# Performance work log

Measured on AMD Instinct MI355X. Metric: run time of the kernel, lower is better.

## Reference

```python
import jax, jax.numpy as jnp
import numpy as np

K = 32
D = 64
N_ITER = 10


def setup_inputs() -> dict:
    key = jax.random.key(0)
    k1, k2 = jax.random.split(key)
    B = 65536
    x = jax.random.normal(k1, (B, D), dtype=jnp.float32)
    c = jnp.zeros((K,), dtype=jnp.float32)
    mu = jax.random.normal(k2, (K, D), dtype=jnp.float32) * 0.1
    A = jnp.tile(jnp.eye(D, dtype=jnp.float32)[None], (K, 1, 1))
    alpha = jnp.float32(0.1)
    return {"x": x, "c": c, "mu": mu, "A": A, "alpha": alpha}


def _grad_phi(x, c, mu, A):
    # Precision matrices Sigma_i^{-1} = A_i^T A_i : (k, d, d)
    P = jnp.einsum('kji,kjl->kil', A, A)
    diff = x[:, None, :] - mu[None, :, :]          # (B, k, d)
    Pd = jnp.einsum('kij,bkj->bki', P, diff)       # Sigma^{-1} (x - mu)
    quad = jnp.einsum('bki,bki->bk', diff, Pd)     # (B, k)
    # Analytic gradient of phi(x) = logsumexp_i(c_i - 0.5 q_i):
    # grad = -sum_i softmax_i(c_i - 0.5 q_i) * Sigma_i^{-1}(x - mu_i)
    w = jax.nn.softmax(c[None, :] - 0.5 * quad, axis=1)  # (B, k)
    return -jnp.einsum('bk,bki->bi', w, Pd)


def reference(x, c, mu, A, alpha):
    def step(x_cur, _):
        x_new = x_cur + alpha * _grad_phi(x_cur, c, mu, A)
        return x_new, None
    x_final, _ = jax.lax.scan(step, x, None, length=N_ITER)
    return x_final
```

## Files before the change

kernel.cpp:

```cpp
#include <hip/hip_runtime.h>
#include <hip/hip_bf16.h>


typedef __attribute__((ext_vector_type(4))) float f32x4;
typedef __attribute__((ext_vector_type(16))) float f32x16;
typedef __attribute__((ext_vector_type(8))) short bf16x8;

#define KC 32
#define NITER 10
#define WAVE_SCR 6144

typedef __attribute__((address_space(3))) void as3_void;
typedef __attribute__((address_space(1))) const void as1_cvoid;

static __device__ __forceinline__ void gl_lds16(const void* g, void* l) {
  __builtin_amdgcn_global_load_lds((as1_cvoid*)g, (as3_void*)l, 16, 0, 0);
}

static __device__ __forceinline__ unsigned pk_bf16(float a, float b) {
  __hip_bfloat16 ha = __float2bfloat16(a), hb = __float2bfloat16(b);
  unsigned short ua = *(unsigned short*)&ha, ub = *(unsigned short*)&hb;
  return (unsigned)ua | ((unsigned)ub << 16);
}

__global__ void precompute1(const float* __restrict__ A, const float* __restrict__ mu,
                            const float* __restrict__ c,
                            float* __restrict__ Pmu_g, float* __restrict__ e_g,
                            __hip_bfloat16* __restrict__ Psw) {
  __shared__ float Pk[64 * 64];
  __shared__ float Pmu_s[64];
  const int k = blockIdx.x, tid = threadIdx.x;
  const float* Ak = A + k * 4096;
  for (int idx = tid; idx < 4096; idx += 256) {
    int i = idx >> 6, l = idx & 63;
    float s = 0.f;
    for (int j = 0; j < 64; ++j) s += Ak[j * 64 + i] * Ak[j * 64 + l];
    Pk[idx] = s;
  }
  __syncthreads();
  if (tid < 64) {
    float s = 0.f;
    for (int l = 0; l < 64; ++l) s += Pk[tid * 64 + l] * mu[k * 64 + l];
    Pmu_s[tid] = s;
    Pmu_g[k * 64 + tid] = s;
  }
  __syncthreads();
  if (tid == 0) {
    float s = 0.f;
    for (int i = 0; i < 64; ++i) s += mu[k * 64 + i] * Pmu_s[i];
    e_g[k] = c[k] - 0.5f * s;
  }
  for (int idx = tid; idx < 4096; idx += 256) {
    int f = idx >> 9, lane = (idx >> 3) & 63, j = idx & 7;
    int mt = f >> 2, kf = f & 3, h = lane >> 5, l5 = lane & 31;
    float v = Pk[(kf * 16 + h * 8 + j) * 64 + mt * 32 + l5];
    Psw[k * 4096 + idx] = __float2bfloat16(v);
  }
}

__global__ void precompute2(const float* __restrict__ Pmu_g,
                            __hip_bfloat16* __restrict__ PmuA,
                            __hip_bfloat16* __restrict__ PmuB) {
  const int tid = threadIdx.x;
  for (int idx = tid; idx < 2048; idx += 256) {
    int f = idx >> 9, lane = (idx >> 3) & 63, j = idx & 7;
    int h = lane >> 5, l5 = lane & 31;
    PmuA[idx] = __float2bfloat16(Pmu_g[l5 * 64 + f * 16 + h * 8 + j]);
  }
  for (int idx = tid; idx < 2048; idx += 256) {
    int f = idx >> 9, lane = (idx >> 3) & 63, j = idx & 7;
    int mt = f >> 1, kf = f & 1, h = lane >> 5, l5 = lane & 31;
    PmuB[idx] = __float2bfloat16(Pmu_g[(kf * 16 + h * 8 + j) * 64 + mt * 32 + l5]);
  }
}

__launch_bounds__(256, 2)
__global__ void denoise_main(const float* __restrict__ x_in,
                             const float* __restrict__ e_g,
                             const float* __restrict__ alpha_g,
                             const __hip_bfloat16* __restrict__ Psw,
                             const __hip_bfloat16* __restrict__ PmuA,
                             const __hip_bfloat16* __restrict__ PmuB,
                             float* __restrict__ out) {
  __shared__ __attribute__((aligned(16))) char pbuf[2 * 8192];
  __shared__ __attribute__((aligned(16))) char scratch[4 * WAVE_SCR];

  const int tid = threadIdx.x;
  const int wave = tid >> 6, lane = tid & 63;
  const int h = lane >> 5, l5 = lane & 31;
  const int base_pt = blockIdx.x * 128 + wave * 32;
  const int pt = base_pt + l5;
  const float alpha = alpha_g[0];

  char* sw = scratch + wave * WAVE_SCR;
  float* pmxw = (float*)sw;
  __hip_bfloat16* wtw = (__hip_bfloat16*)(sw + 4096);

  const bf16x8* PmuAF = (const bf16x8*)PmuA;
  const bf16x8* PmuBF = (const bf16x8*)PmuB;

  float xm[2][16];
#pragma unroll
  for (int mt = 0; mt < 2; ++mt)
#pragma unroll
    for (int rq = 0; rq < 4; ++rq) {
      f32x4 v = *(const f32x4*)&x_in[pt * 64 + mt * 32 + rq * 8 + h * 4];
#pragma unroll
      for (int r = 0; r < 4; ++r) xm[mt][rq * 4 + r] = v[r];
    }

  const f32x16 Z16 = {0.f};

#pragma unroll 1
  for (int it = 0; it < NITER; ++it) {
#pragma unroll
    for (int mt = 0; mt < 2; ++mt)
#pragma unroll
      for (int rq = 0; rq < 4; ++rq) {
        unsigned u0 = pk_bf16(xm[mt][rq * 4 + 0], xm[mt][rq * 4 + 1]);
        unsigned u1 = pk_bf16(xm[mt][rq * 4 + 2], xm[mt][rq * 4 + 3]);
        int blk = mt * 4 + rq;
        int addr = l5 * 128 + (((blk) ^ (l5 & 7)) << 4) + 8 * h;
        uint2 v; v.x = u0; v.y = u1;
        *(uint2*)(sw + addr) = v;
      }

    bf16x8 bx[4];
#pragma unroll
    for (int kf = 0; kf < 4; ++kf) {
      int blk = 2 * kf + h;
      bx[kf] = *(const bf16x8*)(sw + l5 * 128 + ((blk ^ (l5 & 7)) << 4));
    }

    {
      const char* g = (const char*)Psw + wave * 2048 + lane * 16;
      char* l = pbuf + wave * 2048;
      gl_lds16(g, l);
      gl_lds16(g + 1024, l + 1024);
    }

    {
      f32x16 acc = Z16;
#pragma unroll
      for (int kf = 0; kf < 4; ++kf)
        acc = __builtin_amdgcn_mfma_f32_32x32x16_bf16(PmuAF[kf * 64 + lane], bx[kf], acc, 0, 0, 0);
#pragma unroll
      for (int r = 0; r < 16; ++r) {
        int cl = (r & 3) + 8 * (r >> 2) + 4 * h;
        pmxw[cl * 32 + l5] = acc[r];
      }
    }

    float accY[2][16];
#pragma unroll
    for (int mt = 0; mt < 2; ++mt)
#pragma unroll
      for (int r = 0; r < 16; ++r) accY[mt][r] = 0.f;
    float lsum = 0.f;

#pragma unroll 2
    for (int k = 0; k < KC; ++k) {
      __syncthreads();
      if (k < KC - 1) {
        const char* g = (const char*)Psw + (k + 1) * 8192 + wave * 2048 + lane * 16;
        char* l = pbuf + ((k + 1) & 1) * 8192 + wave * 2048;
        gl_lds16(g, l);
        gl_lds16(g + 1024, l + 1024);
      }

      const char* pb = pbuf + (k & 1) * 8192;
      f32x16 y[2];
#pragma unroll
      for (int mt = 0; mt < 2; ++mt) {
        f32x16 acc = Z16;
#pragma unroll
        for (int kf = 0; kf < 4; ++kf)
          acc = __builtin_amdgcn_mfma_f32_32x32x16_bf16(
              *(const bf16x8*)(pb + (mt * 4 + kf) * 1024 + lane * 16), bx[kf], acc, 0, 0, 0);
        y[mt] = acc;
      }

      float p0 = 0.f, p1 = 0.f, p2 = 0.f, p3 = 0.f;
#pragma unroll
      for (int r = 0; r < 16; r += 4) {
        p0 += xm[0][r + 0] * y[0][r + 0] + xm[1][r + 0] * y[1][r + 0];
        p1 += xm[0][r + 1] * y[0][r + 1] + xm[1][r + 1] * y[1][r + 1];
        p2 += xm[0][r + 2] * y[0][r + 2] + xm[1][r + 2] * y[1][r + 2];
        p3 += xm[0][r + 3] * y[0][r + 3] + xm[1][r + 3] * y[1][r + 3];
      }
      float xy = (p0 + p1) + (p2 + p3);
      xy += __shfl_xor(xy, 32, 64);

      const float pk = pmxw[k * 32 + l5];
      const float w = __expf(e_g[k] + pk - 0.5f * xy);
      lsum += w;
      if (h == 0) wtw[l5 * 32 + k] = __float2bfloat16(w);
#pragma unroll
      for (int mt = 0; mt < 2; ++mt)
#pragma unroll
        for (int r = 0; r < 16; ++r) accY[mt][r] += w * y[mt][r];
    }

    bf16x8 wtf[2];
#pragma unroll
    for (int kf = 0; kf < 2; ++kf)
      wtf[kf] = *(const bf16x8*)&wtw[l5 * 32 + kf * 16 + h * 8];
    const float cc = alpha / lsum;
#pragma unroll
    for (int mt = 0; mt < 2; ++mt) {
      f32x16 acc = Z16;
      acc = __builtin_amdgcn_mfma_f32_32x32x16_bf16(PmuBF[(mt * 2 + 0) * 64 + lane], wtf[0], acc, 0, 0, 0);
      acc = __builtin_amdgcn_mfma_f32_32x32x16_bf16(PmuBF[(mt * 2 + 1) * 64 + lane], wtf[1], acc, 0, 0, 0);
#pragma unroll
      for (int r = 0; r < 16; ++r)
        xm[mt][r] += cc * (acc[r] - accY[mt][r]);
    }
  }

#pragma unroll
  for (int mt = 0; mt < 2; ++mt)
#pragma unroll
    for (int rq = 0; rq < 4; ++rq) {
      f32x4 v;
#pragma unroll
      for (int r = 0; r < 4; ++r) v[r] = xm[mt][rq * 4 + r];
      *(f32x4*)&out[pt * 64 + mt * 32 + rq * 8 + h * 4] = v;
    }
}

extern "C" void kernel_launch(void* const* d_in, const int* in_sizes, int n_in,
                              void* d_out, int out_size, void* d_ws, size_t ws_size,
                              hipStream_t stream) {
  (void)in_sizes; (void)n_in; (void)out_size; (void)ws_size;
  const float* x = (const float*)d_in[0];
  const float* c = (const float*)d_in[1];
  const float* mu = (const float*)d_in[2];
  const float* A = (const float*)d_in[3];
  const float* alpha = (const float*)d_in[4];
  float* out = (float*)d_out;

  char* ws = (char*)d_ws;
  float* Pmu_g = (float*)(ws);
  float* e_g = (float*)(ws + 8192);
  __hip_bfloat16* PmuA = (__hip_bfloat16*)(ws + 8448);
  __hip_bfloat16* PmuB = (__hip_bfloat16*)(ws + 12544);
  __hip_bfloat16* Psw = (__hip_bfloat16*)(ws + 16640);

  precompute1<<<32, 256, 0, stream>>>(A, mu, c, Pmu_g, e_g, Psw);
  precompute2<<<1, 256, 0, stream>>>(Pmu_g, PmuA, PmuB);
  denoise_main<<<512, 256, 0, stream>>>(x, e_g, alpha, Psw, PmuA, PmuB, out);
}
```

Before: 313.6 us.

## Load precision matrices directly into registers, drop LDS staging and barriers

Replaces the double-buffered global-to-LDS staging of each component's bf16 precision matrix with direct per-lane global loads into a register double buffer, which removes the per-component __syncthreads. The per-component constant e_k is folded into the stored Pmu·x values ahead of the loop. The two MFMA chains are interleaved and the dot products use explicit FMAs. This raises register pressure (16 extra bf16x8 vectors per lane) and leans on L1/L2 to serve the repeated 256KB Psw reads, with a risk of spills or lower occupancy under launch_bounds(256,2). The wrap-around prefetch on the last iteration loads component 0 again, which is harmless extra traffic.

```diff
diff --git a/kernel.cpp b/kernel.cpp
--- a/kernel.cpp
+++ b/kernel.cpp
@@ -9,13 +9,6 @@
 #define KC 32
 #define NITER 10
 #define WAVE_SCR 6144
-
-typedef __attribute__((address_space(3))) void as3_void;
-typedef __attribute__((address_space(1))) const void as1_cvoid;
-
-static __device__ __forceinline__ void gl_lds16(const void* g, void* l) {
-  __builtin_amdgcn_global_load_lds((as1_cvoid*)g, (as3_void*)l, 16, 0, 0);
-}
 
 static __device__ __forceinline__ unsigned pk_bf16(float a, float b) {
   __hip_bfloat16 ha = __float2bfloat16(a), hb = __float2bfloat16(b);
@@ -82,7 +75,6 @@
                              const __hip_bfloat16* __restrict__ PmuA,
                              const __hip_bfloat16* __restrict__ PmuB,
                              float* __restrict__ out) {
-  __shared__ __attribute__((aligned(16))) char pbuf[2 * 8192];
   __shared__ __attribute__((aligned(16))) char scratch[4 * WAVE_SCR];
 
   const int tid = threadIdx.x;
@@ -96,6 +88,7 @@
   float* pmxw = (float*)sw;
   __hip_bfloat16* wtw = (__hip_bfloat16*)(sw + 4096);
 
+  const bf16x8* PswF = (const bf16x8*)Psw;
   const bf16x8* PmuAF = (const bf16x8*)PmuA;
   const bf16x8* PmuBF = (const bf16x8*)PmuB;
 
@@ -108,6 +101,10 @@
 #pragma unroll
       for (int r = 0; r < 4; ++r) xm[mt][rq * 4 + r] = v[r];
     }
+
+  float ev[16];
+#pragma unroll
+  for (int r = 0; r < 16; ++r) ev[r] = e_g[(r & 3) + 8 * (r >> 2) + 4 * h];
 
   const f32x16 Z16 = {0.f};
 
@@ -120,7 +117,7 @@
         unsigned u0 = pk_bf16(xm[mt][rq * 4 + 0], xm[mt][rq * 4 + 1]);
         unsigned u1 = pk_bf16(xm[mt][rq * 4 + 2], xm[mt][rq * 4 + 3]);
         int blk = mt * 4 + rq;
-        int addr = l5 * 128 + (((blk) ^ (l5 & 7)) << 4) + 8 * h;
+        int addr = l5 * 128 + ((blk ^ (l5 & 7)) << 4) + 8 * h;
         uint2 v; v.x = u0; v.y = u1;
         *(uint2*)(sw + addr) = v;
       }
@@ -132,12 +129,9 @@
       bx[kf] = *(const bf16x8*)(sw + l5 * 128 + ((blk ^ (l5 & 7)) << 4));
     }
 
-    {
-      const char* g = (const char*)Psw + wave * 2048 + lane * 16;
-      char* l = pbuf + wave * 2048;
-      gl_lds16(g, l);
-      gl_lds16(g + 1024, l + 1024);
-    }
+    bf16x8 ap[2][8];
+#pragma unroll
+    for (int f = 0; f < 8; ++f) ap[0][f] = PswF[f * 64 + lane];
 
     {
       f32x16 acc = Z16;
@@ -147,7 +141,7 @@
 #pragma unroll
       for (int r = 0; r < 16; ++r) {
         int cl = (r & 3) + 8 * (r >> 2) + 4 * h;
-        pmxw[cl * 32 + l5] = acc[r];
+        pmxw[cl * 32 + l5] = acc[r] + ev[r];
       }
     }
 
@@ -160,45 +154,47 @@
 
 #pragma unroll 2
     for (int k = 0; k < KC; ++k) {
-      __syncthreads();
-      if (k < KC - 1) {
-        const char* g = (const char*)Psw + (k + 1) * 8192 + wave * 2048 + lane * 16;
-        char* l = pbuf + ((k + 1) & 1) * 8192 + wave * 2048;
-        gl_lds16(g, l);
-        gl_lds16(g + 1024, l + 1024);
-      }
-
-      const char* pb = pbuf + (k & 1) * 8192;
-      f32x16 y[2];
-#pragma unroll
-      for (int mt = 0; mt < 2; ++mt) {
-        f32x16 acc = Z16;
-#pragma unroll
-        for (int kf = 0; kf < 4; ++kf)
-          acc = __builtin_amdgcn_mfma_f32_32x32x16_bf16(
-              *(const bf16x8*)(pb + (mt * 4 + kf) * 1024 + lane * 16), bx[kf], acc, 0, 0, 0);
-        y[mt] = acc;
-      }
-
-      float p0 = 0.f, p1 = 0.f, p2 = 0.f, p3 = 0.f;
+      const int cur = k & 1, nxt = cur ^ 1;
+      const int kn = (k + 1) & (KC - 1);
+#pragma unroll
+      for (int f = 0; f < 8; ++f)
+        ap[nxt][f] = PswF[kn * 512 + f * 64 + lane];
+
+      f32x16 y0 = __builtin_amdgcn_mfma_f32_32x32x16_bf16(ap[cur][0], bx[0], Z16, 0, 0, 0);
+      f32x16 y1 = __builtin_amdgcn_mfma_f32_32x32x16_bf16(ap[cur][4], bx[0], Z16, 0, 0, 0);
+#pragma unroll
+      for (int kf = 1; kf < 4; ++kf) {
+        y0 = __builtin_amdgcn_mfma_f32_32x32x16_bf16(ap[cur][kf], bx[kf], y0, 0, 0, 0);
+        y1 = __builtin_amdgcn_mfma_f32_32x32x16_bf16(ap[cur][4 + kf], bx[kf], y1, 0, 0, 0);
+      }
+
+      float p0 = xm[0][0] * y0[0], p1 = xm[0][1] * y0[1];
+      float p2 = xm[0][2] * y0[2], p3 = xm[0][3] * y0[3];
+#pragma unroll
+      for (int r = 4; r < 16; r += 4) {
+        p0 = fmaf(xm[0][r + 0], y0[r + 0], p0);
+        p1 = fmaf(xm[0][r + 1], y0[r + 1], p1);
+        p2 = fmaf(xm[0][r + 2], y0[r + 2], p2);
+        p3 = fmaf(xm[0][r + 3], y0[r + 3], p3);
+      }
 #pragma unroll
       for (int r = 0; r < 16; r += 4) {
-        p0 += xm[0][r + 0] * y[0][r + 0] + xm[1][r + 0] * y[1][r + 0];
-        p1 += xm[0][r + 1] * y[0][r + 1] + xm[1][r + 1] * y[1][r + 1];
-        p2 += xm[0][r + 2] * y[0][r + 2] + xm[1][r + 2] * y[1][r + 2];
-        p3 += xm[0][r + 3] * y[0][r + 3] + xm[1][r + 3] * y[1][r + 3];
+        p0 = fmaf(xm[1][r + 0], y1[r + 0], p0);
+        p1 = fmaf(xm[1][r + 1], y1[r + 1], p1);
+        p2 = fmaf(xm[1][r + 2], y1[r + 2], p2);
+        p3 = fmaf(xm[1][r + 3], y1[r + 3], p3);
       }
       float xy = (p0 + p1) + (p2 + p3);
       xy += __shfl_xor(xy, 32, 64);
 
-      const float pk = pmxw[k * 32 + l5];
-      const float w = __expf(e_g[k] + pk - 0.5f * xy);
+      const float w = __expf(fmaf(-0.5f, xy, pmxw[k * 32 + l5]));
       lsum += w;
       if (h == 0) wtw[l5 * 32 + k] = __float2bfloat16(w);
 #pragma unroll
-      for (int mt = 0; mt < 2; ++mt)
-#pragma unroll
-        for (int r = 0; r < 16; ++r) accY[mt][r] += w * y[mt][r];
+      for (int r = 0; r < 16; ++r) {
+        accY[0][r] = fmaf(w, y0[r], accY[0][r]);
+        accY[1][r] = fmaf(w, y1[r], accY[1][r]);
+      }
     }
 
     bf16x8 wtf[2];
@@ -208,8 +204,7 @@
     const float cc = alpha / lsum;
 #pragma unroll
     for (int mt = 0; mt < 2; ++mt) {
-      f32x16 acc = Z16;
-      acc = __builtin_amdgcn_mfma_f32_32x32x16_bf16(PmuBF[(mt * 2 + 0) * 64 + lane], wtf[0], acc, 0, 0, 0);
+      f32x16 acc = __builtin_amdgcn_mfma_f32_32x32x16_bf16(PmuBF[(mt * 2 + 0) * 64 + lane], wtf[0], Z16, 0, 0, 0);
       acc = __builtin_amdgcn_mfma_f32_32x32x16_bf16(PmuBF[(mt * 2 + 1) * 64 + lane], wtf[1], acc, 0, 0, 0);
 #pragma unroll
       for (int r = 0; r < 16; ++r)
```

Result: slower. 340.9 us (+8.7%).
